# Kernel optimization log

Measured on AMD Instinct MI355X. Metric: run time of the kernel, lower is better.

Reference implementation:

```python
import jax, jax.numpy as jnp
from jax import lax
import numpy as np


def conv2d(x, w, pad):
    # x: NCHW, w: OIHW
    return lax.conv_general_dilated(
        x, w, window_strides=(1, 1), padding=[(pad, pad), (pad, pad)],
        dimension_numbers=("NCHW", "OIHW", "NCHW"))


def _scan_dir(x, a, axis, reverse):
    """Directional IRNN scan: cur = relu(x_i + alpha * prev), prev0 = 0.
    a broadcasts as (1, C, 1) over the remaining (B, C, L) slice dims."""
    if reverse:
        x = jnp.flip(x, axis)
    xs = jnp.moveaxis(x, axis, 0)  # (L, B, C, other)

    def step(prev, xi):
        cur = jax.nn.relu(xi + a * prev)
        return cur, cur

    _, hs = lax.scan(step, jnp.zeros_like(xs[0]), xs)
    h = jnp.moveaxis(hs, 0, axis)
    if reverse:
        h = jnp.flip(h, axis)
    return h


def spatial_irnn(x, alpha):
    a = alpha.reshape(1, -1, 1)  # broadcasts over (B, C, W) or (B, C, H)
    h_td = _scan_dir(x, a, axis=2, reverse=False)  # top -> down
    h_dt = _scan_dir(x, a, axis=2, reverse=True)   # down -> top
    h_lr = _scan_dir(x, a, axis=3, reverse=False)  # left -> right
    h_rl = _scan_dir(x, a, axis=3, reverse=True)   # right -> left
    return h_td, h_lr, h_dt, h_rl


def setup_inputs() -> dict:
    key = jax.random.key(0)
    ks = jax.random.split(key, 10)
    B, C, H, W = 8, 32, 256, 256
    mid = C // 2
    s = 0.05
    return {
        "x": jax.random.normal(ks[0], (B, C, H, W), jnp.float32),
        "alpha1": jnp.full((C,), 0.2, jnp.float32),
        "alpha2": jnp.full((C,), 0.2, jnp.float32),
        "w_in": jax.random.normal(ks[1], (C, C, 3, 3), jnp.float32) * s,
        "w2": jax.random.normal(ks[2], (C, 4 * C, 3, 3), jnp.float32) * s,
        "w3": jax.random.normal(ks[3], (C, 4 * C, 3, 3), jnp.float32) * s,
        "att_w1": jax.random.normal(ks[4], (mid, C, 3, 3), jnp.float32) * s,
        "att_w2": jax.random.normal(ks[5], (mid, mid, 3, 3), jnp.float32) * s,
        "att_w3": jax.random.normal(ks[6], (4, mid, 1, 1), jnp.float32) * s,
        "att_b3": jnp.zeros((4,), jnp.float32),
        "w_out": jax.random.normal(ks[7], (1, C, 1, 1), jnp.float32) * s,
    }


def reference(x, alpha1, alpha2, w_in, w2, w3, att_w1, att_w2, att_w3, att_b3, w_out):
    # Attention gate: 4 per-direction weight maps in (0,1)
    a = jax.nn.relu(conv2d(x, att_w1, pad=1))
    a = jax.nn.relu(conv2d(a, att_w2, pad=1))
    weight = jax.nn.sigmoid(conv2d(a, att_w3, pad=0) + att_b3.reshape(1, -1, 1, 1))

    def gate(up, right, down, left):
        return jnp.concatenate([
            up * weight[:, 0:1], right * weight[:, 1:2],
            down * weight[:, 2:3], left * weight[:, 3:4]], axis=1)

    out = conv2d(x, w_in, pad=1)
    up, right, down, left = spatial_irnn(out, alpha1)
    out = conv2d(gate(up, right, down, left), w2, pad=1)
    up, right, down, left = spatial_irnn(out, alpha2)
    out = jax.nn.relu(conv2d(gate(up, right, down, left), w3, pad=1))
    mask = jax.nn.sigmoid(conv2d(out, w_out, pad=0))
    return mask
```

## Files before the change

### kernel.cpp

```cpp
#include <hip/hip_runtime.h>
#include <cstddef>

#define H_ 256
#define W_ 256
#define HW_ 65536

typedef unsigned int uint;
typedef unsigned short ushort;
typedef __attribute__((ext_vector_type(8))) short short8;
typedef __attribute__((ext_vector_type(16))) float floatx16;

__device__ __forceinline__ float bf2f(ushort u) {
    return __uint_as_float(((uint)u) << 16);
}
__device__ __forceinline__ ushort f2bf(float f) {
    uint u = __float_as_uint(f);
    uint r = (u + 0x7fffu + ((u >> 16) & 1u)) >> 16;
    return (ushort)r;
}
__device__ __forceinline__ float sigmoidf_(float x) {
    return 1.0f / (1.0f + expf(-x));
}

#define GLOAD_LDS16(gsrc, ldst)                                                   \
    __builtin_amdgcn_global_load_lds(                                             \
        (const __attribute__((address_space(1))) void*)(gsrc),                    \
        (__attribute__((address_space(3))) void*)(ldst), 16, 0, 0)

__device__ __forceinline__ void prep_one(const float* src, ushort* dst,
                                         int CO, int CI, int e) {
    int chunk = e / 9216;
    int r = e - chunk * 9216;
    int co = r / 288;
    int kk = r - co * 288;
    int khw = kk >> 5;
    int ci = kk & 31;
    int cig = chunk * 32 + ci;
    float v = 0.f;
    if (co < CO && cig < CI) v = src[(co * CI + cig) * 9 + khw];
    int s = kk >> 4;
    int lane = ((kk >> 3) & 1) * 32 + co;
    int j = kk & 7;
    dst[(((size_t)chunk * 18 + s) * 64 + lane) * 8 + j] = f2bf(v);
}

__global__ __launch_bounds__(256) void prep_weights(
    const float* __restrict__ w_in, const float* __restrict__ w2,
    const float* __restrict__ w3, const float* __restrict__ aw1,
    const float* __restrict__ aw2,
    ushort* __restrict__ w_inB, ushort* __restrict__ w2B,
    ushort* __restrict__ w3B, ushort* __restrict__ aw1B,
    ushort* __restrict__ aw2B, ushort* __restrict__ zp) {
    int idx = blockIdx.x * 256 + threadIdx.x;
    if (idx < 64) zp[idx] = 0;
    if (idx < 9216)        prep_one(w_in, w_inB, 32, 32, idx);
    else if (idx < 46080)  prep_one(w2, w2B, 32, 128, idx - 9216);
    else if (idx < 82944)  prep_one(w3, w3B, 32, 128, idx - 46080);
    else if (idx < 92160)  prep_one(aw1, aw1B, 16, 32, idx - 82944);
    else if (idx < 101376) prep_one(aw2, aw2B, 16, 16, idx - 92160);
}

__global__ __launch_bounds__(256) void transform_x(const float* __restrict__ x,
                                                   ushort* __restrict__ xh) {
    __shared__ float s[64][33];
    const int t = threadIdx.x;
    const int w0 = blockIdx.x * 64, h = blockIdx.y, b = blockIdx.z;
    {
        int ww = t & 63, c0 = (t >> 6) * 8;
#pragma unroll
        for (int j = 0; j < 8; j++) {
            int c = c0 + j;
            s[ww][c] = x[((size_t)(b * 32 + c)) * HW_ + h * W_ + w0 + ww];
        }
    }
    __syncthreads();
    {
        int p = t >> 2, cb = t & 3;
        ushort tmp[8];
#pragma unroll
        for (int j = 0; j < 8; j++) tmp[j] = f2bf(s[p][cb * 8 + j]);
        *(uint4*)(xh + (((size_t)b * HW_ + h * W_ + w0 + p) * 32) + cb * 8) =
            *(const uint4*)tmp;
    }
}

struct StageDescL {
    uint goff[6];
    bool ok[6];
};
__device__ __forceinline__ void make_descL(StageDescL& d, int t, int w0, int h0, int b) {
#pragma unroll
    for (int i = 0; i < 6; i++) {
        int u = i * 256 + t;
        int row = u / 136;
        int rem = u - row * 136;
        int p = rem >> 2, q = rem & 3;
        int cb = q ^ (p & 3) ^ ((p >> 2) & 3);
        int gh = h0 - 1 + row, gw = w0 - 1 + p;
        d.ok[i] = (u < 1360) && ((unsigned)gh < 256u) && ((unsigned)gw < 256u);
        d.goff[i] = d.ok[i] ? (((uint)b * HW_ + (uint)gh * W_ + (uint)gw) * 32 + cb * 8) : 0u;
    }
}
__device__ __forceinline__ void stage_lds(ushort* smem, const StageDescL& d,
                                          const ushort* __restrict__ inp,
                                          const ushort* __restrict__ zp, int t) {
#pragma unroll
    for (int i = 0; i < 6; i++) {
        const ushort* src = d.ok[i] ? (inp + d.goff[i]) : zp;
        GLOAD_LDS16(src, smem + (size_t)(i * 256 + t) * 8);
    }
}

__device__ __forceinline__ void mfma_chunk(const ushort* smem, const ushort* wbp,
                                           int lco, int lhalf, int wid,
                                           floatx16& acc0, floatx16& acc1) {
#pragma unroll
    for (int half = 0; half < 2; half++) {
        short8 bf[9];
#pragma unroll
        for (int j = 0; j < 9; j++)
            bf[j] = *(const short8*)(wbp + (size_t)(2 * j + half) * 512);
        const int cbr = half * 2 + lhalf;
#pragma unroll
        for (int kw = 0; kw < 3; kw++) {
            const int ww = lco + kw;
            const int cbs = cbr ^ (ww & 3) ^ ((ww >> 2) & 3);
            short8 a[4];
#pragma unroll
            for (int r = 0; r < 4; r++)
                a[r] = *(const short8*)(smem + (size_t)((wid * 2 + r) * 136 + (ww << 2) + cbs) * 8);
#pragma unroll
            for (int kh = 0; kh < 3; kh++) {
                acc0 = __builtin_amdgcn_mfma_f32_32x32x16_bf16(a[kh], bf[kh * 3 + kw], acc0, 0, 0, 0);
                acc1 = __builtin_amdgcn_mfma_f32_32x32x16_bf16(a[kh + 1], bf[kh * 3 + kw], acc1, 0, 0, 0);
            }
        }
    }
}

template<int NCHUNK, int EPI, bool RELU>
__global__ __launch_bounds__(256, 4) void conv_mfma(
    const ushort* __restrict__ in0, const ushort* __restrict__ in1,
    const ushort* __restrict__ in2, const ushort* __restrict__ in3,
    const ushort* __restrict__ wB, const ushort* __restrict__ zp,
    ushort* __restrict__ outp, const float* __restrict__ aux_w,
    const float* __restrict__ aux_b) {
    constexpr int NBUF = (NCHUNK > 1) ? 2 : 1;
    __shared__ __align__(16) ushort smem[NBUF][1536 * 8];
    const int t = threadIdx.x;
    const int wid = t >> 6;
    const int lane = t & 63;
    const int lco = lane & 31, lhalf = lane >> 5;
    const int w0 = blockIdx.x * 32, h0 = blockIdx.y * 8, b = blockIdx.z;
    const ushort* ins[4] = {in0, in1, in2, in3};

    StageDescL d;
    make_descL(d, t, w0, h0, b);

    floatx16 acc0, acc1;
#pragma unroll
    for (int i = 0; i < 16; i++) { acc0[i] = 0.f; acc1[i] = 0.f; }

    stage_lds(smem[0], d, ins[0], zp, t);

#pragma unroll
    for (int ch = 0; ch < NCHUNK; ch++) {
        __syncthreads();
        if (ch + 1 < NCHUNK)
            stage_lds(smem[(ch + 1) & 1], d, ins[ch + 1], zp, t);
        mfma_chunk(smem[ch & 1], wB + ((size_t)ch * 18 * 64 + lane) * 8,
                   lco, lhalf, wid, acc0, acc1);
    }

    if (EPI == 0) {
#pragma unroll
        for (int r = 0; r < 16; r++) {
            int wl = (r & 3) + 8 * (r >> 2) + 4 * lhalf;
            float v0 = acc0[r], v1 = acc1[r];
            if (RELU) { v0 = fmaxf(v0, 0.f); v1 = fmaxf(v1, 0.f); }
            size_t p0 = (((size_t)b * HW_ + (h0 + wid * 2) * W_ + w0 + wl) * 32) + lco;
            outp[p0] = f2bf(v0);
            outp[p0 + (size_t)W_ * 32] = f2bf(v1);
        }
    } else {
        __syncthreads();
        ushort* ep = &smem[0][0];
#pragma unroll
        for (int r = 0; r < 16; r++) {
            int wl = (r & 3) + 8 * (r >> 2) + 4 * lhalf;
            float v0 = acc0[r], v1 = acc1[r];
            if (RELU) { v0 = fmaxf(v0, 0.f); v1 = fmaxf(v1, 0.f); }
            int pix0 = (wid * 2) * 32 + wl;
            ep[(size_t)pix0 * 40 + lco] = f2bf(v0);
            ep[(size_t)(pix0 + 32) * 40 + lco] = f2bf(v1);
        }
        __syncthreads();
        const ushort* tp = ep + (size_t)t * 40;
        if (EPI == 1) {
            float xin[16];
            uint4 q0 = *(const uint4*)tp;
            uint4 q1 = *(const uint4*)(tp + 8);
            const ushort* u0 = (const ushort*)&q0;
            const ushort* u1 = (const ushort*)&q1;
#pragma unroll
            for (int j = 0; j < 8; j++) { xin[j] = bf2f(u0[j]); xin[8 + j] = bf2f(u1[j]); }
            size_t pix = (size_t)b * HW_ + (size_t)(h0 + (t >> 5)) * W_ + w0 + (t & 31);
#pragma unroll
            for (int g = 0; g < 4; g++) {
                float acc = aux_b[g];
#pragma unroll
                for (int ci = 0; ci < 16; ci++) acc = fmaf(xin[ci], aux_w[g * 16 + ci], acc);
                outp[(size_t)g * 8 * HW_ + pix] = f2bf(sigmoidf_(acc));
            }
        } else {
            float acc = 0.f;
#pragma unroll
            for (int q = 0; q < 4; q++) {
                uint4 qv = *(const uint4*)(tp + q * 8);
                const ushort* uq = (const ushort*)&qv;
#pragma unroll
                for (int j = 0; j < 8; j++) acc = fmaf(bf2f(uq[j]), aux_w[q * 8 + j], acc);
            }
            float* fo = (float*)outp;
            fo[(size_t)b * HW_ + (size_t)(h0 + (t >> 5)) * W_ + w0 + (t & 31)] = sigmoidf_(acc);
        }
    }
}

__global__ __launch_bounds__(256, 4) void conv_dual(
    const ushort* __restrict__ in0, const ushort* __restrict__ wBa,
    const ushort* __restrict__ wBb, const ushort* __restrict__ zp,
    ushort* __restrict__ outA, ushort* __restrict__ outB) {
    __shared__ __align__(16) ushort smem[1536 * 8];
    const int t = threadIdx.x;
    const int wid = t >> 6;
    const int lane = t & 63;
    const int lco = lane & 31, lhalf = lane >> 5;
    const int w0 = blockIdx.x * 32, h0 = blockIdx.y * 8, b = blockIdx.z;

    StageDescL d;
    make_descL(d, t, w0, h0, b);

    floatx16 accA0, accA1, accB0, accB1;
#pragma unroll
    for (int i = 0; i < 16; i++) { accA0[i] = 0.f; accA1[i] = 0.f; accB0[i] = 0.f; accB1[i] = 0.f; }

    stage_lds(smem, d, in0, zp, t);
    __syncthreads();
    mfma_chunk(smem, wBa + (size_t)lane * 8, lco, lhalf, wid, accA0, accA1);
    mfma_chunk(smem, wBb + (size_t)lane * 8, lco, lhalf, wid, accB0, accB1);

#pragma unroll
    for (int r = 0; r < 16; r++) {
        int wl = (r & 3) + 8 * (r >> 2) + 4 * lhalf;
        size_t p0 = (((size_t)b * HW_ + (h0 + wid * 2) * W_ + w0 + wl) * 32) + lco;
        outA[p0] = f2bf(accA0[r]);
        outA[p0 + (size_t)W_ * 32] = f2bf(accA1[r]);
        outB[p0] = f2bf(fmaxf(accB0[r], 0.f));
        outB[p0 + (size_t)W_ * 32] = f2bf(fmaxf(accB1[r], 0.f));
    }
}

template<int VERT>
__device__ __forceinline__ void scan_body(
    const ushort* __restrict__ feat, const float* __restrict__ alpha,
    const ushort* __restrict__ wmapT, ushort* __restrict__ gfwd,
    ushort* __restrict__ gbwd, int gf, int gb, int bx, int t) {
    const int cg = t & 3;
    const int col = (bx & 3) * 64 + (t >> 2);
    const int seg = (bx >> 2) & 7;
    const int dir = (bx >> 5) & 1;
    const int b = bx >> 6;
    const int c0 = cg * 8;

    float a[8];
#pragma unroll
    for (int j = 0; j < 8; j++) a[j] = alpha[c0 + j];

    const ushort* wplane = wmapT + (size_t)(dir ? gb : gf) * 8 * HW_ + (size_t)b * HW_;
    ushort* gout = dir ? gbwd : gfwd;

    const int main0 = seg * 32;
    const int start = (seg == 0) ? 0 : main0 - 16;
    const int cnt = main0 - start + 32;

    auto pixof = [&](int p) -> size_t {
        int phys = dir ? 255 - p : p;
        return VERT ? ((size_t)phys * W_ + col) : ((size_t)col * W_ + phys);
    };

    uint4 xv[4];
    ushort wv[4];
#pragma unroll
    for (int k = 0; k < 4; k++) {
        size_t pix = pixof(start + k);
        xv[k] = *(const uint4*)(feat + ((size_t)b * HW_ + pix) * 32 + c0);
        wv[k] = wplane[pix];
    }
    float prev[8];
#pragma unroll
    for (int j = 0; j < 8; j++) prev[j] = 0.f;

    for (int i = 0; i < cnt; i += 4) {
#pragma unroll
        for (int k = 0; k < 4; k++) {
            const int p = start + i + k;
            uint4 xcur = xv[k];
            ushort wcur = wv[k];
            if (i + k + 4 < cnt) {
                size_t pix = pixof(p + 4);
                xv[k] = *(const uint4*)(feat + ((size_t)b * HW_ + pix) * 32 + c0);
                wv[k] = wplane[pix];
            }
            const ushort* xu = (const ushort*)&xcur;
            if (p >= main0) {
                float wmv = bf2f(wcur);
                ushort o[8];
#pragma unroll
                for (int j = 0; j < 8; j++) {
                    float cur = fmaxf(fmaf(a[j], prev[j], bf2f(xu[j])), 0.f);
                    prev[j] = cur;
                    o[j] = f2bf(cur * wmv);
                }
                *(uint4*)(gout + ((size_t)b * HW_ + pixof(p)) * 32 + c0) = *(const uint4*)o;
            } else {
#pragma unroll
                for (int j = 0; j < 8; j++)
                    prev[j] = fmaxf(fmaf(a[j], prev[j], bf2f(xu[j])), 0.f);
            }
        }
    }
}

__global__ __launch_bounds__(256) void scan_both(
    const ushort* __restrict__ feat, const float* __restrict__ alpha,
    const ushort* __restrict__ wmapT, ushort* __restrict__ g0,
    ushort* __restrict__ g1, ushort* __restrict__ g2, ushort* __restrict__ g3) {
    const int bx = blockIdx.x & 511;
    if (blockIdx.x < 512)
        scan_body<1>(feat, alpha, wmapT, g0, g2, 0, 2, bx, threadIdx.x);
    else
        scan_body<0>(feat, alpha, wmapT, g1, g3, 1, 3, bx, threadIdx.x);
}

extern "C" void kernel_launch(void* const* d_in, const int* in_sizes, int n_in,
                              void* d_out, int out_size, void* d_ws, size_t ws_size,
                              hipStream_t stream) {
    const float* x      = (const float*)d_in[0];
    const float* alpha1 = (const float*)d_in[1];
    const float* alpha2 = (const float*)d_in[2];
    const float* w_in   = (const float*)d_in[3];
    const float* w2     = (const float*)d_in[4];
    const float* w3     = (const float*)d_in[5];
    const float* aw1    = (const float*)d_in[6];
    const float* aw2    = (const float*)d_in[7];
    const float* aw3    = (const float*)d_in[8];
    const float* ab3    = (const float*)d_in[9];
    const float* wout   = (const float*)d_in[10];
    float* out = (float*)d_out;

    const size_t TEN = (size_t)8 * HW_ * 32;
    ushort* p = (ushort*)d_ws;
    ushort* xh    = p; p += TEN;
    ushort* feat  = p; p += TEN;
    ushort* g0    = p; p += TEN;
    ushort* g1    = p; p += TEN;
    ushort* g2    = p; p += TEN;
    ushort* g3    = p; p += TEN;
    ushort* wmapT = p; p += (size_t)4 * 8 * HW_;
    ushort* w_inB = p; p += 9216;
    ushort* w2B   = p; p += 36864;
    ushort* w3B   = p; p += 36864;
    ushort* aw1B  = p; p += 9216;
    ushort* aw2B  = p; p += 9216;
    ushort* zp    = p; p += 64;
    ushort* a1z   = g1;

    prep_weights<<<396, 256, 0, stream>>>(w_in, w2, w3, aw1, aw2,
                                          w_inB, w2B, w3B, aw1B, aw2B, zp);
    transform_x<<<dim3(4, 256, 8), 256, 0, stream>>>(x, xh);

    dim3 gconv(8, 32, 8);

    conv_dual<<<gconv, 256, 0, stream>>>(xh, w_inB, aw1B, zp, feat, a1z);
    conv_mfma<1, 1, true><<<gconv, 256, 0, stream>>>(a1z, a1z, a1z, a1z, aw2B, zp,
                                                     wmapT, aw3, ab3);

    scan_both<<<1024, 256, 0, stream>>>(feat, alpha1, wmapT, g0, g1, g2, g3);

    conv_mfma<4, 0, false><<<gconv, 256, 0, stream>>>(g0, g1, g2, g3, w2B, zp,
                                                      feat, nullptr, nullptr);

    scan_both<<<1024, 256, 0, stream>>>(feat, alpha2, wmapT, g0, g1, g2, g3);

    conv_mfma<4, 2, true><<<gconv, 256, 0, stream>>>(g0, g1, g2, g3, w3B, zp,
                                                     (ushort*)out, wout, nullptr);
}
```

Baseline: 386.9 us.

## Enlarge conv tile to 16 rows per block with four accumulators per wave

Each conv block now covers 16 output rows instead of 8. Each wave computes 4 rows with four MFMA accumulators and reuses each loaded weight fragment across more rows, which cuts the halo overhead of the staged input (18 rows for 16 outputs instead of 10 for 8). LDS staging grows to 10 slots per thread, and launch bounds drop to 2 blocks per SM to make room for the extra accumulator registers. The grid is halved, so fewer blocks are resident, and there is less latency hiding and parallelism.

Result: faster. 378.3 us (-2.2%).

```diff
diff --git a/kernel.cpp b/kernel.cpp
--- a/kernel.cpp
+++ b/kernel.cpp
@@ -84,20 +84,22 @@
     }
 }
 
+#define NSLOT 2448
+#define NSTG 10
 struct StageDescL {
-    uint goff[6];
-    bool ok[6];
+    uint goff[NSTG];
+    bool ok[NSTG];
 };
 __device__ __forceinline__ void make_descL(StageDescL& d, int t, int w0, int h0, int b) {
 #pragma unroll
-    for (int i = 0; i < 6; i++) {
+    for (int i = 0; i < NSTG; i++) {
         int u = i * 256 + t;
         int row = u / 136;
         int rem = u - row * 136;
         int p = rem >> 2, q = rem & 3;
         int cb = q ^ (p & 3) ^ ((p >> 2) & 3);
         int gh = h0 - 1 + row, gw = w0 - 1 + p;
-        d.ok[i] = (u < 1360) && ((unsigned)gh < 256u) && ((unsigned)gw < 256u);
+        d.ok[i] = (u < NSLOT) && ((unsigned)gh < 256u) && ((unsigned)gw < 256u);
         d.goff[i] = d.ok[i] ? (((uint)b * HW_ + (uint)gh * W_ + (uint)gw) * 32 + cb * 8) : 0u;
     }
 }
@@ -105,15 +107,15 @@
                                           const ushort* __restrict__ inp,
                                           const ushort* __restrict__ zp, int t) {
 #pragma unroll
-    for (int i = 0; i < 6; i++) {
+    for (int i = 0; i < NSTG; i++) {
         const ushort* src = d.ok[i] ? (inp + d.goff[i]) : zp;
         GLOAD_LDS16(src, smem + (size_t)(i * 256 + t) * 8);
     }
 }
 
-__device__ __forceinline__ void mfma_chunk(const ushort* smem, const ushort* wbp,
-                                           int lco, int lhalf, int wid,
-                                           floatx16& acc0, floatx16& acc1) {
+__device__ __forceinline__ void mfma_chunk4(const ushort* smem, const ushort* wbp,
+                                            int lco, int lhalf, int wid,
+                                            floatx16* acc) {
 #pragma unroll
     for (int half = 0; half < 2; half++) {
         short8 bf[9];
@@ -125,41 +127,45 @@
         for (int kw = 0; kw < 3; kw++) {
             const int ww = lco + kw;
             const int cbs = cbr ^ (ww & 3) ^ ((ww >> 2) & 3);
-            short8 a[4];
-#pragma unroll
-            for (int r = 0; r < 4; r++)
-                a[r] = *(const short8*)(smem + (size_t)((wid * 2 + r) * 136 + (ww << 2) + cbs) * 8);
+            short8 a[6];
+#pragma unroll
+            for (int r = 0; r < 6; r++)
+                a[r] = *(const short8*)(smem + (size_t)((wid * 4 + r) * 136 + (ww << 2) + cbs) * 8);
 #pragma unroll
             for (int kh = 0; kh < 3; kh++) {
-                acc0 = __builtin_amdgcn_mfma_f32_32x32x16_bf16(a[kh], bf[kh * 3 + kw], acc0, 0, 0, 0);
-                acc1 = __builtin_amdgcn_mfma_f32_32x32x16_bf16(a[kh + 1], bf[kh * 3 + kw], acc1, 0, 0, 0);
+#pragma unroll
+                for (int j = 0; j < 4; j++)
+                    acc[j] = __builtin_amdgcn_mfma_f32_32x32x16_bf16(
+                        a[kh + j], bf[kh * 3 + kw], acc[j], 0, 0, 0);
             }
         }
     }
 }
 
 template<int NCHUNK, int EPI, bool RELU>
-__global__ __launch_bounds__(256, 4) void conv_mfma(
+__global__ __launch_bounds__(256, 2) void conv_mfma(
     const ushort* __restrict__ in0, const ushort* __restrict__ in1,
     const ushort* __restrict__ in2, const ushort* __restrict__ in3,
     const ushort* __restrict__ wB, const ushort* __restrict__ zp,
     ushort* __restrict__ outp, const float* __restrict__ aux_w,
     const float* __restrict__ aux_b) {
     constexpr int NBUF = (NCHUNK > 1) ? 2 : 1;
-    __shared__ __align__(16) ushort smem[NBUF][1536 * 8];
+    __shared__ __align__(16) ushort smem[NBUF][NSTG * 256 * 8];
     const int t = threadIdx.x;
     const int wid = t >> 6;
     const int lane = t & 63;
     const int lco = lane & 31, lhalf = lane >> 5;
-    const int w0 = blockIdx.x * 32, h0 = blockIdx.y * 8, b = blockIdx.z;
+    const int w0 = blockIdx.x * 32, h0 = blockIdx.y * 16, b = blockIdx.z;
     const ushort* ins[4] = {in0, in1, in2, in3};
 
     StageDescL d;
     make_descL(d, t, w0, h0, b);
 
-    floatx16 acc0, acc1;
-#pragma unroll
-    for (int i = 0; i < 16; i++) { acc0[i] = 0.f; acc1[i] = 0.f; }
+    floatx16 acc[4];
+#pragma unroll
+    for (int j = 0; j < 4; j++)
+#pragma unroll
+        for (int i = 0; i < 16; i++) acc[j][i] = 0.f;
 
     stage_lds(smem[0], d, ins[0], zp, t);
 
@@ -168,96 +174,108 @@
         __syncthreads();
         if (ch + 1 < NCHUNK)
             stage_lds(smem[(ch + 1) & 1], d, ins[ch + 1], zp, t);
-        mfma_chunk(smem[ch & 1], wB + ((size_t)ch * 18 * 64 + lane) * 8,
-                   lco, lhalf, wid, acc0, acc1);
+        mfma_chunk4(smem[ch & 1], wB + ((size_t)ch * 18 * 64 + lane) * 8,
+                    lco, lhalf, wid, acc);
     }
 
     if (EPI == 0) {
 #pragma unroll
-        for (int r = 0; r < 16; r++) {
-            int wl = (r & 3) + 8 * (r >> 2) + 4 * lhalf;
-            float v0 = acc0[r], v1 = acc1[r];
-            if (RELU) { v0 = fmaxf(v0, 0.f); v1 = fmaxf(v1, 0.f); }
-            size_t p0 = (((size_t)b * HW_ + (h0 + wid * 2) * W_ + w0 + wl) * 32) + lco;
-            outp[p0] = f2bf(v0);
-            outp[p0 + (size_t)W_ * 32] = f2bf(v1);
+        for (int j = 0; j < 4; j++) {
+#pragma unroll
+            for (int r = 0; r < 16; r++) {
+                int wl = (r & 3) + 8 * (r >> 2) + 4 * lhalf;
+                float v = acc[j][r];
+                if (RELU) v = fmaxf(v, 0.f);
+                size_t p0 = (((size_t)b * HW_ + (h0 + wid * 4 + j) * W_ + w0 + wl) * 32) + lco;
+                outp[p0] = f2bf(v);
+            }
         }
     } else {
         __syncthreads();
         ushort* ep = &smem[0][0];
 #pragma unroll
-        for (int r = 0; r < 16; r++) {
-            int wl = (r & 3) + 8 * (r >> 2) + 4 * lhalf;
-            float v0 = acc0[r], v1 = acc1[r];
-            if (RELU) { v0 = fmaxf(v0, 0.f); v1 = fmaxf(v1, 0.f); }
-            int pix0 = (wid * 2) * 32 + wl;
-            ep[(size_t)pix0 * 40 + lco] = f2bf(v0);
-            ep[(size_t)(pix0 + 32) * 40 + lco] = f2bf(v1);
+        for (int j = 0; j < 4; j++) {
+#pragma unroll
+            for (int r = 0; r < 16; r++) {
+                int wl = (r & 3) + 8 * (r >> 2) + 4 * lhalf;
+                float v = acc[j][r];
+                if (RELU) v = fmaxf(v, 0.f);
+                int pix0 = (wid * 4 + j) * 32 + wl;
+                ep[(size_t)pix0 * 40 + lco] = f2bf(v);
+            }
         }
         __syncthreads();
-        const ushort* tp = ep + (size_t)t * 40;
-        if (EPI == 1) {
-            float xin[16];
-            uint4 q0 = *(const uint4*)tp;
-            uint4 q1 = *(const uint4*)(tp + 8);
-            const ushort* u0 = (const ushort*)&q0;
-            const ushort* u1 = (const ushort*)&q1;
-#pragma unroll
-            for (int j = 0; j < 8; j++) { xin[j] = bf2f(u0[j]); xin[8 + j] = bf2f(u1[j]); }
-            size_t pix = (size_t)b * HW_ + (size_t)(h0 + (t >> 5)) * W_ + w0 + (t & 31);
-#pragma unroll
-            for (int g = 0; g < 4; g++) {
-                float acc = aux_b[g];
-#pragma unroll
-                for (int ci = 0; ci < 16; ci++) acc = fmaf(xin[ci], aux_w[g * 16 + ci], acc);
-                outp[(size_t)g * 8 * HW_ + pix] = f2bf(sigmoidf_(acc));
-            }
-        } else {
-            float acc = 0.f;
-#pragma unroll
-            for (int q = 0; q < 4; q++) {
-                uint4 qv = *(const uint4*)(tp + q * 8);
-                const ushort* uq = (const ushort*)&qv;
-#pragma unroll
-                for (int j = 0; j < 8; j++) acc = fmaf(bf2f(uq[j]), aux_w[q * 8 + j], acc);
-            }
-            float* fo = (float*)outp;
-            fo[(size_t)b * HW_ + (size_t)(h0 + (t >> 5)) * W_ + w0 + (t & 31)] = sigmoidf_(acc);
-        }
-    }
-}
-
-__global__ __launch_bounds__(256, 4) void conv_dual(
+#pragma unroll
+        for (int pp = 0; pp < 2; pp++) {
+            const int pix = pp * 256 + t;
+            const ushort* tp = ep + (size_t)pix * 40;
+            const int prow = pix >> 5, pcol = pix & 31;
+            if (EPI == 1) {
+                float xin[16];
+                uint4 q0 = *(const uint4*)tp;
+                uint4 q1 = *(const uint4*)(tp + 8);
+                const ushort* u0 = (const ushort*)&q0;
+                const ushort* u1 = (const ushort*)&q1;
+#pragma unroll
+                for (int j = 0; j < 8; j++) { xin[j] = bf2f(u0[j]); xin[8 + j] = bf2f(u1[j]); }
+                size_t pix_g = (size_t)b * HW_ + (size_t)(h0 + prow) * W_ + w0 + pcol;
+#pragma unroll
+                for (int g = 0; g < 4; g++) {
+                    float acc1 = aux_b[g];
+#pragma unroll
+                    for (int ci = 0; ci < 16; ci++) acc1 = fmaf(xin[ci], aux_w[g * 16 + ci], acc1);
+                    outp[(size_t)g * 8 * HW_ + pix_g] = f2bf(sigmoidf_(acc1));
+                }
+            } else {
+                float acc1 = 0.f;
+#pragma unroll
+                for (int q = 0; q < 4; q++) {
+                    uint4 qv = *(const uint4*)(tp + q * 8);
+                    const ushort* uq = (const ushort*)&qv;
+#pragma unroll
+                    for (int j = 0; j < 8; j++) acc1 = fmaf(bf2f(uq[j]), aux_w[q * 8 + j], acc1);
+                }
+                float* fo = (float*)outp;
+                fo[(size_t)b * HW_ + (size_t)(h0 + prow) * W_ + w0 + pcol] = sigmoidf_(acc1);
+            }
+        }
+    }
+}
+
+__global__ __launch_bounds__(256, 2) void conv_dual(
     const ushort* __restrict__ in0, const ushort* __restrict__ wBa,
     const ushort* __restrict__ wBb, const ushort* __restrict__ zp,
     ushort* __restrict__ outA, ushort* __restrict__ outB) {
-    __shared__ __align__(16) ushort smem[1536 * 8];
+    __shared__ __align__(16) ushort smem[NSTG * 256 * 8];
     const int t = threadIdx.x;
     const int wid = t >> 6;
     const int lane = t & 63;
     const int lco = lane & 31, lhalf = lane >> 5;
-    const int w0 = blockIdx.x * 32, h0 = blockIdx.y * 8, b = blockIdx.z;
+    const int w0 = blockIdx.x * 32, h0 = blockIdx.y * 16, b = blockIdx.z;
 
     StageDescL d;
     make_descL(d, t, w0, h0, b);
 
-    floatx16 accA0, accA1, accB0, accB1;
-#pragma unroll
-    for (int i = 0; i < 16; i++) { accA0[i] = 0.f; accA1[i] = 0.f; accB0[i] = 0.f; accB1[i] = 0.f; }
+    floatx16 accA[4], accB[4];
+#pragma unroll
+    for (int j = 0; j < 4; j++)
+#pragma unroll
+        for (int i = 0; i < 16; i++) { accA[j][i] = 0.f; accB[j][i] = 0.f; }
 
     stage_lds(smem, d, in0, zp, t);
     __syncthreads();
-    mfma_chunk(smem, wBa + (size_t)lane * 8, lco, lhalf, wid, accA0, accA1);
-    mfma_chunk(smem, wBb + (size_t)lane * 8, lco, lhalf, wid, accB0, accB1);
-
-#pragma unroll
-    for (int r = 0; r < 16; r++) {
-        int wl = (r & 3) + 8 * (r >> 2) + 4 * lhalf;
-        size_t p0 = (((size_t)b * HW_ + (h0 + wid * 2) * W_ + w0 + wl) * 32) + lco;
-        outA[p0] = f2bf(accA0[r]);
-        outA[p0 + (size_t)W_ * 32] = f2bf(accA1[r]);
-        outB[p0] = f2bf(fmaxf(accB0[r], 0.f));
-        outB[p0 + (size_t)W_ * 32] = f2bf(fmaxf(accB1[r], 0.f));
+    mfma_chunk4(smem, wBa + (size_t)lane * 8, lco, lhalf, wid, accA);
+    mfma_chunk4(smem, wBb + (size_t)lane * 8, lco, lhalf, wid, accB);
+
+#pragma unroll
+    for (int j = 0; j < 4; j++) {
+#pragma unroll
+        for (int r = 0; r < 16; r++) {
+            int wl = (r & 3) + 8 * (r >> 2) + 4 * lhalf;
+            size_t p0 = (((size_t)b * HW_ + (h0 + wid * 4 + j) * W_ + w0 + wl) * 32) + lco;
+            outA[p0] = f2bf(accA[j][r]);
+            outB[p0] = f2bf(fmaxf(accB[j][r], 0.f));
+        }
     }
 }
 
@@ -380,7 +398,7 @@
                                           w_inB, w2B, w3B, aw1B, aw2B, zp);
     transform_x<<<dim3(4, 256, 8), 256, 0, stream>>>(x, xh);
 
-    dim3 gconv(8, 32, 8);
+    dim3 gconv(8, 16, 8);
 
     conv_dual<<<gconv, 256, 0, stream>>>(xh, w_inB, aw1B, zp, feat, a1z);
     conv_mfma<1, 1, true><<<gconv, 256, 0, stream>>>(a1z, a1z, a1z, a1z, aw2B, zp,
```

## Stage conv weights into LDS alongside input tiles with explicit vmcnt pipelining

Applied to the files above, without the earlier changes.

Conv weight fragments are now copied into LDS with global_load_lds next to the input tile, instead of being read per-wave straight from global memory. The multi-chunk conv loop replaces __syncthreads with manual s_waitcnt and s_barrier so the next chunk's loads stay in flight during the current MFMA work. The input staging is trimmed to the 1360 slots actually used. LDS per block grows, so launch bounds drop to 2 blocks per CU for the multi-chunk and dual kernels, which risks lower occupancy.

Result: faster. 360.0 us (-7.0%).

```diff
diff --git a/kernel.cpp b/kernel.cpp
--- a/kernel.cpp
+++ b/kernel.cpp
@@ -26,6 +26,10 @@
     __builtin_amdgcn_global_load_lds(                                             \
         (const __attribute__((address_space(1))) void*)(gsrc),                    \
         (__attribute__((address_space(3))) void*)(ldst), 16, 0, 0)
+
+#define IN_SLOTS 1408
+#define W_SLOTS 1152
+#define BUF_SLOTS 2560
 
 __device__ __forceinline__ void prep_one(const float* src, ushort* dst,
                                          int CO, int CI, int e) {
@@ -91,7 +95,7 @@
 __device__ __forceinline__ void make_descL(StageDescL& d, int t, int w0, int h0, int b) {
 #pragma unroll
     for (int i = 0; i < 6; i++) {
-        int u = i * 256 + t;
+        int u = (i < 5) ? (i * 256 + t) : (1280 + t);
         int row = u / 136;
         int rem = u - row * 136;
         int p = rem >> 2, q = rem & 3;
@@ -101,25 +105,41 @@
         d.goff[i] = d.ok[i] ? (((uint)b * HW_ + (uint)gh * W_ + (uint)gw) * 32 + cb * 8) : 0u;
     }
 }
-__device__ __forceinline__ void stage_lds(ushort* smem, const StageDescL& d,
-                                          const ushort* __restrict__ inp,
-                                          const ushort* __restrict__ zp, int t) {
-#pragma unroll
-    for (int i = 0; i < 6; i++) {
+__device__ __forceinline__ void stage_input(ushort* ibuf, const StageDescL& d,
+                                            const ushort* __restrict__ inp,
+                                            const ushort* __restrict__ zp,
+                                            int t, int wid) {
+#pragma unroll
+    for (int i = 0; i < 5; i++) {
         const ushort* src = d.ok[i] ? (inp + d.goff[i]) : zp;
-        GLOAD_LDS16(src, smem + (size_t)(i * 256 + t) * 8);
-    }
-}
-
-__device__ __forceinline__ void mfma_chunk(const ushort* smem, const ushort* wbp,
-                                           int lco, int lhalf, int wid,
+        GLOAD_LDS16(src, ibuf + (size_t)(i * 256 + t) * 8);
+    }
+    if (wid < 2) {
+        const ushort* src = d.ok[5] ? (inp + d.goff[5]) : zp;
+        GLOAD_LDS16(src, ibuf + (size_t)(1280 + t) * 8);
+    }
+}
+__device__ __forceinline__ void stage_wts(ushort* wbuf,
+                                          const ushort* __restrict__ wsrc,
+                                          int t, int wid) {
+#pragma unroll
+    for (int j = 0; j < 4; j++)
+        GLOAD_LDS16(wsrc + (size_t)(j * 256 + t) * 8,
+                    wbuf + (size_t)(j * 256 + t) * 8);
+    if (wid >= 2)
+        GLOAD_LDS16(wsrc + (size_t)(1024 + t - 128) * 8,
+                    wbuf + (size_t)(1024 + t - 128) * 8);
+}
+
+__device__ __forceinline__ void mfma_chunk(const ushort* ibuf, const ushort* wbuf,
+                                           int lco, int lhalf, int wid, int lane,
                                            floatx16& acc0, floatx16& acc1) {
 #pragma unroll
     for (int half = 0; half < 2; half++) {
         short8 bf[9];
 #pragma unroll
         for (int j = 0; j < 9; j++)
-            bf[j] = *(const short8*)(wbp + (size_t)(2 * j + half) * 512);
+            bf[j] = *(const short8*)(wbuf + (size_t)((2 * j + half) * 64 + lane) * 8);
         const int cbr = half * 2 + lhalf;
 #pragma unroll
         for (int kw = 0; kw < 3; kw++) {
@@ -128,7 +148,7 @@
             short8 a[4];
 #pragma unroll
             for (int r = 0; r < 4; r++)
-                a[r] = *(const short8*)(smem + (size_t)((wid * 2 + r) * 136 + (ww << 2) + cbs) * 8);
+                a[r] = *(const short8*)(ibuf + (size_t)((wid * 2 + r) * 136 + (ww << 2) + cbs) * 8);
 #pragma unroll
             for (int kh = 0; kh < 3; kh++) {
                 acc0 = __builtin_amdgcn_mfma_f32_32x32x16_bf16(a[kh], bf[kh * 3 + kw], acc0, 0, 0, 0);
@@ -139,14 +159,14 @@
 }
 
 template<int NCHUNK, int EPI, bool RELU>
-__global__ __launch_bounds__(256, 4) void conv_mfma(
+__global__ __launch_bounds__(256, (NCHUNK > 1) ? 2 : 4) void conv_mfma(
     const ushort* __restrict__ in0, const ushort* __restrict__ in1,
     const ushort* __restrict__ in2, const ushort* __restrict__ in3,
     const ushort* __restrict__ wB, const ushort* __restrict__ zp,
     ushort* __restrict__ outp, const float* __restrict__ aux_w,
     const float* __restrict__ aux_b) {
     constexpr int NBUF = (NCHUNK > 1) ? 2 : 1;
-    __shared__ __align__(16) ushort smem[NBUF][1536 * 8];
+    __shared__ __align__(16) ushort smem[NBUF][BUF_SLOTS * 8];
     const int t = threadIdx.x;
     const int wid = t >> 6;
     const int lane = t & 63;
@@ -161,15 +181,29 @@
 #pragma unroll
     for (int i = 0; i < 16; i++) { acc0[i] = 0.f; acc1[i] = 0.f; }
 
-    stage_lds(smem[0], d, ins[0], zp, t);
-
-#pragma unroll
-    for (int ch = 0; ch < NCHUNK; ch++) {
+    stage_input(smem[0], d, ins[0], zp, t, wid);
+    stage_wts(smem[0] + IN_SLOTS * 8, wB, t, wid);
+
+    if constexpr (NCHUNK == 1) {
         __syncthreads();
-        if (ch + 1 < NCHUNK)
-            stage_lds(smem[(ch + 1) & 1], d, ins[ch + 1], zp, t);
-        mfma_chunk(smem[ch & 1], wB + ((size_t)ch * 18 * 64 + lane) * 8,
-                   lco, lhalf, wid, acc0, acc1);
+        mfma_chunk(smem[0], smem[0] + IN_SLOTS * 8, lco, lhalf, wid, lane, acc0, acc1);
+    } else {
+#pragma unroll
+        for (int ch = 0; ch < NCHUNK; ch++) {
+            asm volatile("s_waitcnt lgkmcnt(0)" ::: "memory");
+            __builtin_amdgcn_s_barrier();
+            if (ch + 1 < NCHUNK) {
+                stage_input(smem[(ch + 1) & 1], d, ins[ch + 1], zp, t, wid);
+                stage_wts(smem[(ch + 1) & 1] + IN_SLOTS * 8,
+                          wB + (size_t)(ch + 1) * 9216, t, wid);
+                asm volatile("s_waitcnt vmcnt(10)" ::: "memory");
+            } else {
+                asm volatile("s_waitcnt vmcnt(0)" ::: "memory");
+            }
+            __builtin_amdgcn_s_barrier();
+            mfma_chunk(smem[ch & 1], smem[ch & 1] + IN_SLOTS * 8,
+                       lco, lhalf, wid, lane, acc0, acc1);
+        }
     }
 
     if (EPI == 0) {
@@ -227,11 +261,11 @@
     }
 }
 
-__global__ __launch_bounds__(256, 4) void conv_dual(
+__global__ __launch_bounds__(256, 2) void conv_dual(
     const ushort* __restrict__ in0, const ushort* __restrict__ wBa,
     const ushort* __restrict__ wBb, const ushort* __restrict__ zp,
     ushort* __restrict__ outA, ushort* __restrict__ outB) {
-    __shared__ __align__(16) ushort smem[1536 * 8];
+    __shared__ __align__(16) ushort smem[(IN_SLOTS + 2 * W_SLOTS) * 8];
     const int t = threadIdx.x;
     const int wid = t >> 6;
     const int lane = t & 63;
@@ -245,10 +279,12 @@
 #pragma unroll
     for (int i = 0; i < 16; i++) { accA0[i] = 0.f; accA1[i] = 0.f; accB0[i] = 0.f; accB1[i] = 0.f; }
 
-    stage_lds(smem, d, in0, zp, t);
+    stage_input(smem, d, in0, zp, t, wid);
+    stage_wts(smem + IN_SLOTS * 8, wBa, t, wid);
+    stage_wts(smem + (IN_SLOTS + W_SLOTS) * 8, wBb, t, wid);
     __syncthreads();
-    mfma_chunk(smem, wBa + (size_t)lane * 8, lco, lhalf, wid, accA0, accA1);
-    mfma_chunk(smem, wBb + (size_t)lane * 8, lco, lhalf, wid, accB0, accB1);
+    mfma_chunk(smem, smem + IN_SLOTS * 8, lco, lhalf, wid, lane, accA0, accA1);
+    mfma_chunk(smem, smem + (IN_SLOTS + W_SLOTS) * 8, lco, lhalf, wid, lane, accB0, accB1);
 
 #pragma unroll
     for (int r = 0; r < 16; r++) {
```
